# Performance work log

Measured on AMD Instinct MI355X. Metric: run time of the kernel, lower is better.

The kernel has to match this reference:

```python
import jax, jax.numpy as jnp
import numpy as np
from jax import lax

K_NEIGHBORS = 15
LAM = 1.0
EPS = 1e-8


def _cdist(a):
    # Euclidean pairwise distance, safe sqrt (zero diag has zero grad path handled in bwd module too)
    sq = jnp.sum(a * a, axis=1)
    d2 = sq[:, None] + sq[None, :] - 2.0 * (a @ a.T)
    d2 = jnp.maximum(d2, 0.0)
    safe = jnp.where(d2 > 0.0, d2, 1.0)
    return jnp.where(d2 > 0.0, jnp.sqrt(safe), 0.0)


def _knn_loss(z, x, k):
    B = x.shape[0]
    x_dist = _cdist(x)
    z_dist = _cdist(z)
    eye = jnp.eye(B, dtype=bool)
    x_ns = jnp.where(eye, jnp.inf, x_dist)  # fill_diagonal_(inf)
    _, knn_idx = lax.top_k(-x_ns, k)        # k smallest per row
    mask = jnp.zeros((B, B), dtype=bool).at[jnp.arange(B)[:, None], knn_idx].set(True)
    mask = mask | mask.T
    x_max = jnp.max(jnp.where(mask, x_dist, -jnp.inf))
    z_max = jnp.max(jnp.where(mask, z_dist, -jnp.inf))
    x_norm = x_dist / (x_max + EPS)
    z_norm = z_dist / (z_max + EPS)
    diff2 = (z_norm - x_norm) ** 2
    # mean over masked entries == masked_select(...).mean()
    return jnp.sum(jnp.where(mask, diff2, 0.0)) / jnp.sum(mask).astype(diff2.dtype)


def setup_inputs() -> dict:
    key = jax.random.key(0)
    ks = jax.random.split(key, 13)
    D, H1, H2, L = 1024, 2048, 512, 64

    def lin(k, fan_in, fan_out):
        bound = 1.0 / np.sqrt(fan_in)
        kw, kb = jax.random.split(k)
        w = jax.random.uniform(kw, (fan_in, fan_out), jnp.float32, -bound, bound)
        b = jax.random.uniform(kb, (fan_out,), jnp.float32, -bound, bound)
        return w, b

    x = jax.random.normal(ks[0], (8192, D), jnp.float32)
    w_e0, b_e0 = lin(ks[1], D, H1)
    w_e1, b_e1 = lin(ks[2], H1, H2)
    w_e2, b_e2 = lin(ks[3], H2, L)
    w_d0, b_d0 = lin(ks[4], L, H2)
    w_d1, b_d1 = lin(ks[5], H2, H1)
    w_d2, b_d2 = lin(ks[6], H1, D)
    return {"x": x,
            "w_e0": w_e0, "b_e0": b_e0, "w_e1": w_e1, "b_e1": b_e1, "w_e2": w_e2, "b_e2": b_e2,
            "w_d0": w_d0, "b_d0": b_d0, "w_d1": w_d1, "b_d1": b_d1, "w_d2": w_d2, "b_d2": b_d2}


def reference(x, w_e0, b_e0, w_e1, b_e1, w_e2, b_e2, w_d0, b_d0, w_d1, b_d1, w_d2, b_d2):
    h = jax.nn.relu(x @ w_e0 + b_e0)
    h = jax.nn.relu(h @ w_e1 + b_e1)
    z = h @ w_e2 + b_e2
    h = jax.nn.relu(z @ w_d0 + b_d0)
    h = jax.nn.relu(h @ w_d1 + b_d1)
    x_rec = h @ w_d2 + b_d2
    rec_loss = jnp.mean((x_rec - x) ** 2)
    knn_loss = _knn_loss(z, x, K_NEIGHBORS)
    total = rec_loss + LAM * knn_loss
    return (total, z, rec_loss, knn_loss)
```

## Files before the change

kernel.cpp:

```cpp
#include <hip/hip_runtime.h>


typedef __attribute__((ext_vector_type(8))) short bf16x8;
typedef __attribute__((ext_vector_type(4))) float f32x4;

#define DEVINL static __device__ __forceinline__

DEVINL unsigned short f2bf(float f){
  unsigned u = __float_as_uint(f);
  u += 0x7FFFu + ((u >> 16) & 1u);
  return (unsigned short)(u >> 16);
}

DEVINL int med3i(int a, int b, int c){
  int d;
  asm("v_med3_i32 %0, %1, %2, %3" : "=v"(d) : "v"(a), "v"(b), "v"(c));
  return d;
}

DEVINL void gload16(const unsigned short* g, void* lds){
  __builtin_amdgcn_global_load_lds(
      (const __attribute__((address_space(1))) unsigned int*)g,
      (__attribute__((address_space(3))) unsigned int*)lds, 16, 0, 0);
}

DEVINL void lds_barrier(){
  asm volatile("s_waitcnt lgkmcnt(0)" ::: "memory");
  __builtin_amdgcn_s_barrier();
  asm volatile("" ::: "memory");
}

#define NLISTS 39

#define INS15(NAME, R0,R1,R2,R3,R4,R5,R6,R7,R8,R9,R10,R11,R12,R13,R14)  \
  auto NAME = [&](int v){                                               \
    if (v < R14){                                                       \
      R14 = med3i(v, R13, R14); R13 = med3i(v, R12, R13);               \
      R12 = med3i(v, R11, R12); R11 = med3i(v, R10, R11);               \
      R10 = med3i(v, R9 , R10); R9  = med3i(v, R8 , R9 );               \
      R8  = med3i(v, R7 , R8 ); R7  = med3i(v, R6 , R7 );               \
      R6  = med3i(v, R5 , R6 ); R5  = med3i(v, R4 , R5 );               \
      R4  = med3i(v, R3 , R4 ); R3  = med3i(v, R2 , R3 );               \
      R2  = med3i(v, R1 , R2 ); R1  = med3i(v, R0 , R1 );               \
      R0  = min(R0, v);                                                 \
    }                                                                   \
  }

__global__ __launch_bounds__(256) void cvtT_k(const float* __restrict__ x,
    unsigned short* __restrict__ xb, float* __restrict__ xsq,
    const float* __restrict__ w0, const float* __restrict__ w1,
    const float* __restrict__ w2, const float* __restrict__ w3,
    const float* __restrict__ w4, const float* __restrict__ w5,
    unsigned short* __restrict__ t0, unsigned short* __restrict__ t1,
    unsigned short* __restrict__ t2, unsigned short* __restrict__ t3,
    unsigned short* __restrict__ t4, unsigned short* __restrict__ t5)
{
  __shared__ float t[32][33];
  const int tid = threadIdx.x;
  if (blockIdx.x >= 2048){
    int id = blockIdx.x - 2048;
    const float* w; unsigned short* wt; int K, N, loc;
    if      (id < 2048){ w = w0; wt = t0; K = 1024; N = 2048; loc = id; }
    else if (id < 3072){ w = w1; wt = t1; K = 2048; N = 512;  loc = id - 2048; }
    else if (id < 3104){ w = w2; wt = t2; K = 512;  N = 64;   loc = id - 3072; }
    else if (id < 3136){ w = w3; wt = t3; K = 64;   N = 512;  loc = id - 3104; }
    else if (id < 4160){ w = w4; wt = t4; K = 512;  N = 2048; loc = id - 3136; }
    else               { w = w5; wt = t5; K = 2048; N = 1024; loc = id - 4160; }
    const int ntn = N >> 5;
    const int n0 = (loc % ntn) << 5, k0 = (loc / ntn) << 5;
    const int tx = tid & 31, ty = tid >> 5;
    #pragma unroll
    for (int q = 0; q < 4; q++)
      t[ty + 8*q][tx] = w[(size_t)(k0 + ty + 8*q) * N + n0 + tx];
    __syncthreads();
    #pragma unroll
    for (int q = 0; q < 4; q++)
      wt[(size_t)(n0 + ty + 8*q) * K + k0 + tx] = f2bf(t[tx][ty + 8*q]);
    return;
  }
  const int lane = tid & 63, wv = tid >> 6;
  const int row = blockIdx.x * 4 + wv;
  const float4* px = (const float4*)(x + (size_t)row * 1024);
  ushort4* pb = (ushort4*)(xb + (size_t)row * 1024);
  float ss = 0.f;
  #pragma unroll
  for (int q = 0; q < 4; q++){
    float4 v = px[q * 64 + lane];
    ss += v.x*v.x + v.y*v.y + v.z*v.z + v.w*v.w;
    ushort4 o; o.x = f2bf(v.x); o.y = f2bf(v.y); o.z = f2bf(v.z); o.w = f2bf(v.w);
    pb[q * 64 + lane] = o;
  }
  #pragma unroll
  for (int o = 32; o; o >>= 1) ss += __shfl_xor(ss, o);
  if (!lane) xsq[row] = ss;
}

__global__ __launch_bounds__(256, 2) void thr_k(
    const unsigned short* __restrict__ Xb, const float* __restrict__ xsq,
    int* __restrict__ thrI)
{
  __shared__ short As[128][32];
  __shared__ unsigned short d2s[128][130];
  const int tid = threadIdx.x, lane = tid & 63, wid = tid >> 6;
  const int wr = wid >> 1, wc = wid & 1;
  const int r16 = lane & 15, kg = lane >> 4;
  const int srow = lane >> 2, scol = (lane & 3) * 8;
  const float INF = __builtin_inff();
  const int b0 = blockIdx.x * 128;

  float xr[4][4];
  #pragma unroll
  for (int m = 0; m < 4; m++)
    #pragma unroll
    for (int r = 0; r < 4; r++)
      xr[m][r] = xsq[b0 + wr*64 + m*16 + kg*4 + r];

  f32x4 acc[4][4] = {};
  for (int k0 = 0; k0 < 1024; k0 += 32){
    __syncthreads();
    for (int ch = wid; ch < 8; ch += 4)
      gload16(Xb + (size_t)(b0 + ch*16 + srow) * 1024 + k0 + scol, &As[ch*16][0]);
    __syncthreads();
    bf16x8 af[4], bfr[4];
    #pragma unroll
    for (int m = 0; m < 4; m++) af[m]  = *(const bf16x8*)&As[wr*64 + m*16 + r16][kg*8];
    #pragma unroll
    for (int n = 0; n < 4; n++) bfr[n] = *(const bf16x8*)&As[wc*64 + n*16 + r16][kg*8];
    #pragma unroll
    for (int m = 0; m < 4; m++)
      #pragma unroll
      for (int n = 0; n < 4; n++)
        acc[m][n] = __builtin_amdgcn_mfma_f32_16x16x32_bf16(af[m], bfr[n], acc[m][n], 0, 0, 0);
  }
  float xc[4];
  #pragma unroll
  for (int n = 0; n < 4; n++) xc[n] = xsq[b0 + wc*64 + n*16 + r16];
  #pragma unroll
  for (int m = 0; m < 4; m++){
    #pragma unroll
    for (int n = 0; n < 4; n++){
      const int lc = wc*64 + n*16 + r16;
      #pragma unroll
      for (int r = 0; r < 4; r++){
        const int lr = wr*64 + m*16 + kg*4 + r;
        float v = xr[m][r] + xc[n] - 2.f * acc[m][n][r];
        if (lr == lc) v = INF;
        d2s[lr][lc] = f2bf(v);
      }
    }
  }
  __syncthreads();
  if (tid < 128){
    int r0,r1,r2,r3,r4,r5,r6,r7,r8,r9,r10,r11,r12,r13,r14;
    r0=r1=r2=r3=r4=r5=r6=r7=r8=r9=r10=r11=r12=r13=r14=0x7FFFFFFF;
    INS15(ins, r0,r1,r2,r3,r4,r5,r6,r7,r8,r9,r10,r11,r12,r13,r14);
    #pragma unroll 4
    for (int cc = 0; cc < 128; cc += 2){
      unsigned pv = *(const unsigned*)&d2s[tid][cc];
      ins((int)((pv << 16) | (unsigned)cc));
      ins((int)((pv & 0xFFFF0000u) | (unsigned)(cc + 1)));
    }
    thrI[b0 + tid] = (int)(((unsigned)r14 & 0xFFFF0000u) | 0xFFFFu);
  }
}

template<int BM, int BN, int WM, int WN, bool RELU, int OMODE>
__global__ __launch_bounds__(256, 2) void gemm_bt(
    const unsigned short* __restrict__ A, const unsigned short* __restrict__ Bt,
    const float* __restrict__ bias, int M, int N, int K,
    unsigned short* __restrict__ Cb, float* __restrict__ Cf,
    const float* __restrict__ Xref, float* __restrict__ recPart)
{
  constexpr int FM = BM / (WM * 16), FN = BN / (WN * 16);
  __shared__ short As[BM][32];
  __shared__ short Bs[BN][32];
  __shared__ float wsum[4];
  const int tid = threadIdx.x, lane = tid & 63, wid = tid >> 6;
  const int wr = wid / WN, wc = wid % WN;
  const int r16 = lane & 15, kg = lane >> 4;
  const int row0 = blockIdx.x * BM, col0 = blockIdx.y * BN;
  const int srow = lane >> 2, scol = (lane & 3) * 8;
  (void)M;
  f32x4 acc[FM][FN] = {};
  for (int k0 = 0; k0 < K; k0 += 32){
    __syncthreads();
    for (int ch = wid; ch < BM/16; ch += 4)
      gload16(A + (size_t)(row0 + ch*16 + srow) * K + k0 + scol, &As[ch*16][0]);
    for (int ch = wid; ch < BN/16; ch += 4)
      gload16(Bt + (size_t)(col0 + ch*16 + srow) * K + k0 + scol, &Bs[ch*16][0]);
    __syncthreads();
    bf16x8 af[FM], bfr[FN];
    #pragma unroll
    for (int m = 0; m < FM; m++) af[m]  = *(const bf16x8*)&As[wr*FM*16 + m*16 + r16][kg*8];
    #pragma unroll
    for (int n = 0; n < FN; n++) bfr[n] = *(const bf16x8*)&Bs[wc*FN*16 + n*16 + r16][kg*8];
    #pragma unroll
    for (int m = 0; m < FM; m++)
      #pragma unroll
      for (int n = 0; n < FN; n++)
        acc[m][n] = __builtin_amdgcn_mfma_f32_16x16x32_bf16(af[m], bfr[n], acc[m][n], 0, 0, 0);
  }
  float lsum = 0.f;
  #pragma unroll
  for (int m = 0; m < FM; m++){
    #pragma unroll
    for (int n = 0; n < FN; n++){
      const int gc = col0 + wc*FN*16 + n*16 + r16;
      const float bv = bias[gc];
      #pragma unroll
      for (int r = 0; r < 4; r++){
        const int gr = row0 + wr*FM*16 + m*16 + kg*4 + r;
        float v = acc[m][n][r] + bv;
        if (RELU) v = fmaxf(v, 0.f);
        if (OMODE == 2){
          float d = v - Xref[(size_t)gr * N + gc];
          lsum += d * d;
        } else {
          Cb[(size_t)gr * N + gc] = f2bf(v);
          if (OMODE == 1) Cf[(size_t)gr * N + gc] = v;
        }
      }
    }
  }
  if (OMODE == 2){
    #pragma unroll
    for (int o = 32; o; o >>= 1) lsum += __shfl_xor(lsum, o);
    if (!lane) wsum[wid] = lsum;
    __syncthreads();
    if (!tid) recPart[blockIdx.y * gridDim.x + blockIdx.x] =
        wsum[0] + wsum[1] + wsum[2] + wsum[3];
  }
}

__global__ __launch_bounds__(256, 2) void gram_topk_k(
    const unsigned short* __restrict__ Xb, const float* __restrict__ xsq,
    const int* __restrict__ thrI, int* __restrict__ topP,
    const unsigned short* __restrict__ gBt, const float* __restrict__ gBias,
    unsigned short* __restrict__ gC)
{
  __shared__ short As[128][32];
  __shared__ short Bs[128][32];
  __shared__ unsigned short d2s[128][130];
  __shared__ int colL[128][15];
  __shared__ unsigned bkt[16][256];
  const int tid = threadIdx.x, lane = tid & 63, wid = tid >> 6;
  const int wr = wid >> 1, wc = wid & 1;
  const int r16 = lane & 15, kg = lane >> 4;
  const int srow = lane >> 2, scol = (lane & 3) * 8;

  if (blockIdx.x >= 512){
    const int gb = blockIdx.x - 512;
    const int row0 = (gb & 63) * 128, col0 = (gb >> 6) * 128;
    f32x4 acc[4][4] = {};
    for (int k0 = 0; k0 < 1024; k0 += 32){
      __syncthreads();
      for (int ch = wid; ch < 8; ch += 4){
        gload16(Xb  + (size_t)(row0 + ch*16 + srow) * 1024 + k0 + scol, &As[ch*16][0]);
        gload16(gBt + (size_t)(col0 + ch*16 + srow) * 1024 + k0 + scol, &Bs[ch*16][0]);
      }
      __syncthreads();
      bf16x8 af[4], bfr[4];
      #pragma unroll
      for (int m = 0; m < 4; m++) af[m]  = *(const bf16x8*)&As[wr*64 + m*16 + r16][kg*8];
      #pragma unroll
      for (int n = 0; n < 4; n++) bfr[n] = *(const bf16x8*)&Bs[wc*64 + n*16 + r16][kg*8];
      #pragma unroll
      for (int m = 0; m < 4; m++)
        #pragma unroll
        for (int n = 0; n < 4; n++)
          acc[m][n] = __builtin_amdgcn_mfma_f32_16x16x32_bf16(af[m], bfr[n], acc[m][n], 0, 0, 0);
    }
    #pragma unroll
    for (int m = 0; m < 4; m++){
      #pragma unroll
      for (int n = 0; n < 4; n++){
        const int gc = col0 + wc*64 + n*16 + r16;
        const float bv = gBias[gc];
        #pragma unroll
        for (int r = 0; r < 4; r++){
          const int gr = row0 + wr*64 + m*16 + kg*4 + r;
          gC[(size_t)gr * 2048 + gc] = f2bf(fmaxf(acc[m][n][r] + bv, 0.f));
        }
      }
    }
    return;
  }

  const float INF = __builtin_inff();
  const int INFI = 0x7FFFFFFF;
  const int bi = blockIdx.x & 63;
  const int cl = blockIdx.x >> 6;
  const int row0 = bi * 128;
  const int ntt = (cl == 7) ? 5 : 4;
  const int selrow = tid & 127, half = tid >> 7, selc0 = half * 64;
  const int thrRI = thrI[row0 + selrow];

  auto stage = [&](int j0s, int k0s){
    for (int ch = wid; ch < 8; ch += 4){
      gload16(Xb + (size_t)(row0 + ch*16 + srow) * 1024 + k0s + scol, &As[ch*16][0]);
      gload16(Xb + (size_t)(j0s  + ch*16 + srow) * 1024 + k0s + scol, &Bs[ch*16][0]);
    }
  };

  int r0,r1,r2,r3,r4,r5,r6,r7,r8,r9,r10,r11,r12,r13,r14;
  r0=r1=r2=r3=r4=r5=r6=r7=r8=r9=r10=r11=r12=r13=r14=INFI;
  INS15(insR, r0,r1,r2,r3,r4,r5,r6,r7,r8,r9,r10,r11,r12,r13,r14);
  int c0,c1,c2,c3,c4,c5,c6,c7,c8,c9,c10,c11,c12,c13,c14;
  INS15(insC, c0,c1,c2,c3,c4,c5,c6,c7,c8,c9,c10,c11,c12,c13,c14);

  float xr[4][4];
  #pragma unroll
  for (int m = 0; m < 4; m++)
    #pragma unroll
    for (int r = 0; r < 4; r++)
      xr[m][r] = xsq[row0 + wr*64 + m*16 + kg*4 + r];

  stage(((bi + cl * 4) & 63) * 128, 0);

  for (int tt = 0; tt < ntt; ++tt){
    const int d = cl * 4 + tt;
    const int bj = (bi + d) & 63;
    const int j0 = bj * 128;
    f32x4 acc[4][4] = {};
    for (int k0 = 0; k0 < 1024; k0 += 32){
      __syncthreads();
      bf16x8 af[4], bfr[4];
      #pragma unroll
      for (int m = 0; m < 4; m++) af[m]  = *(const bf16x8*)&As[wr*64 + m*16 + r16][kg*8];
      #pragma unroll
      for (int n = 0; n < 4; n++) bfr[n] = *(const bf16x8*)&Bs[wc*64 + n*16 + r16][kg*8];
      __syncthreads();
      if (k0 + 32 < 1024)      stage(j0, k0 + 32);
      else if (tt + 1 < ntt)   stage(((bi + d + 1) & 63) * 128, 0);
      #pragma unroll
      for (int m = 0; m < 4; m++)
        #pragma unroll
        for (int n = 0; n < 4; n++)
          acc[m][n] = __builtin_amdgcn_mfma_f32_16x16x32_bf16(af[m], bfr[n], acc[m][n], 0, 0, 0);
    }
    float xc[4];
    #pragma unroll
    for (int n = 0; n < 4; n++) xc[n] = xsq[j0 + wc*64 + n*16 + r16];
    #pragma unroll
    for (int m = 0; m < 4; m++){
      #pragma unroll
      for (int n = 0; n < 4; n++){
        const int lc = wc*64 + n*16 + r16;
        #pragma unroll
        for (int r = 0; r < 4; r++){
          const int lr = wr*64 + m*16 + kg*4 + r;
          float v = xr[m][r] + xc[n] - 2.f * acc[m][n][r];
          if (row0 + lr == j0 + lc) v = INF;
          d2s[lr][lc] = f2bf(v);
        }
      }
    }
    lds_barrier();

    {
      int cnt = 0;
      const int jg0 = j0 + selc0;
      #pragma unroll 4
      for (int cc = 0; cc < 64; cc += 2){
        unsigned pv = *(const unsigned*)&d2s[selrow][selc0 + cc];
        int p0 = (int)((pv << 16) | (unsigned)(jg0 + cc));
        int p1 = (int)((pv & 0xFFFF0000u) | (unsigned)(jg0 + cc + 1));
        if (p0 <= thrRI){
          if (cnt < 16){ bkt[cnt][tid] = (unsigned)p0; ++cnt; } else insR(p0);
        }
        if (p1 <= thrRI){
          if (cnt < 16){ bkt[cnt][tid] = (unsigned)p1; ++cnt; } else insR(p1);
        }
      }
      for (int q = 0; q < cnt; ++q) insR((int)bkt[q][tid]);
    }

    const bool doCol = (d >= 1) && (d <= 31);
    if (doCol){
      c0=c1=c2=c3=c4=c5=c6=c7=c8=c9=c10=c11=c12=c13=c14=INFI;
      const int thrCI = thrI[j0 + selrow];
      const int rbase = row0 + selc0;
      int cnt = 0;
      #pragma unroll 4
      for (int rr = 0; rr < 64; ++rr){
        unsigned v = d2s[selc0 + rr][selrow];
        int pk = (int)((v << 16) | (unsigned)(rbase + rr));
        if (pk <= thrCI){
          if (cnt < 16){ bkt[cnt][tid] = (unsigned)pk; ++cnt; } else insC(pk);
        }
      }
      for (int q = 0; q < cnt; ++q) insC((int)bkt[q][tid]);
      if (half){
        colL[selrow][0]=c0;  colL[selrow][1]=c1;  colL[selrow][2]=c2;
        colL[selrow][3]=c3;  colL[selrow][4]=c4;  colL[selrow][5]=c5;
        colL[selrow][6]=c6;  colL[selrow][7]=c7;  colL[selrow][8]=c8;
        colL[selrow][9]=c9;  colL[selrow][10]=c10; colL[selrow][11]=c11;
        colL[selrow][12]=c12; colL[selrow][13]=c13; colL[selrow][14]=c14;
      }
    }
    lds_barrier();
    if (doCol && !half){
      #pragma unroll 1
      for (int q = 0; q < 15; ++q){
        int v = colL[selrow][q];
        if (v >= c14) break;
        insC(v);
      }
      int* dst = topP + ((size_t)(j0 + selrow) * NLISTS + (8 + d - 1)) * 15;
      dst[0]=c0;  dst[1]=c1;  dst[2]=c2;  dst[3]=c3;  dst[4]=c4;
      dst[5]=c5;  dst[6]=c6;  dst[7]=c7;  dst[8]=c8;  dst[9]=c9;
      dst[10]=c10; dst[11]=c11; dst[12]=c12; dst[13]=c13; dst[14]=c14;
    }
  }
  lds_barrier();
  if (half){
    colL[selrow][0]=r0;  colL[selrow][1]=r1;  colL[selrow][2]=r2;
    colL[selrow][3]=r3;  colL[selrow][4]=r4;  colL[selrow][5]=r5;
    colL[selrow][6]=r6;  colL[selrow][7]=r7;  colL[selrow][8]=r8;
    colL[selrow][9]=r9;  colL[selrow][10]=r10; colL[selrow][11]=r11;
    colL[selrow][12]=r12; colL[selrow][13]=r13; colL[selrow][14]=r14;
  }
  lds_barrier();
  if (!half){
    #pragma unroll 1
    for (int q = 0; q < 15; ++q){
      int v = colL[selrow][q];
      if (v >= r14) break;
      insR(v);
    }
    int* dst = topP + ((size_t)(row0 + selrow) * NLISTS + cl) * 15;
    dst[0]=r0;  dst[1]=r1;  dst[2]=r2;  dst[3]=r3;  dst[4]=r4;
    dst[5]=r5;  dst[6]=r6;  dst[7]=r7;  dst[8]=r8;  dst[9]=r9;
    dst[10]=r10; dst[11]=r11; dst[12]=r12; dst[13]=r13; dst[14]=r14;
  }
}

__global__ __launch_bounds__(256) void merge_topk_k(const int* __restrict__ topP,
    int* __restrict__ knn, float* __restrict__ d2k, float* __restrict__ xpart)
{
  __shared__ float wmax[4];
  const int lane = threadIdx.x & 63, wid = threadIdx.x >> 6;
  const int row = blockIdx.x * 4 + wid;
  const int* tp = topP + (size_t)row * (NLISTS * 15);
  const int INFI = 0x7FFFFFFF;
  int c0 = tp[lane];
  int c1 = tp[lane + 64];
  int c2 = tp[lane + 128];
  int c3 = tp[lane + 192];
  int c4 = tp[lane + 256];
  int c5 = tp[lane + 320];
  int c6 = tp[lane + 384];
  int c7 = tp[lane + 448];
  int c8 = tp[lane + 512];
  int c9 = (lane < 9) ? tp[lane + 576] : INFI;
  float last = 0.f;
  for (int it = 0; it < 15; ++it){
    int m = min(min(min(c0, c1), min(c2, c3)), min(min(c4, c5), min(c6, c7)));
    m = min(m, min(c8, c9));
    #pragma unroll
    for (int o = 32; o; o >>= 1) m = min(m, __shfl_xor(m, o));
    if (!lane){
      knn[row * 15 + it] = m & 0xFFFF;
      float f = __uint_as_float((unsigned)m & 0xFFFF0000u);
      d2k[row * 15 + it] = f;
      last = f;
    }
    c0 = (c0 == m) ? INFI : c0;   c1 = (c1 == m) ? INFI : c1;
    c2 = (c2 == m) ? INFI : c2;   c3 = (c3 == m) ? INFI : c3;
    c4 = (c4 == m) ? INFI : c4;   c5 = (c5 == m) ? INFI : c5;
    c6 = (c6 == m) ? INFI : c6;   c7 = (c7 == m) ? INFI : c7;
    c8 = (c8 == m) ? INFI : c8;   c9 = (c9 == m) ? INFI : c9;
  }
  if (!lane) wmax[wid] = last;
  __syncthreads();
  if (!threadIdx.x)
    xpart[blockIdx.x] = fmaxf(fmaxf(wmax[0], wmax[1]), fmaxf(wmax[2], wmax[3]));
}

__global__ __launch_bounds__(256) void pair_sums_k(
    const float* __restrict__ z, const int* __restrict__ knn,
    const float* __restrict__ d2k,
    float* __restrict__ zzP, float* __restrict__ zxP, float* __restrict__ xxP,
    float* __restrict__ zmP, float* __restrict__ cntP)
{
  __shared__ float red[4][5];
  const int lane = threadIdx.x & 63, wid = threadIdx.x >> 6;
  float szz = 0.f, szx = 0.f, sxx = 0.f, mz = 0.f, scnt = 0.f;
  for (int p = blockIdx.x * 4 + wid; p < 122880; p += gridDim.x * 4){
    const int i = p / 15;
    const int j = knn[p];
    const float dx2 = d2k[p];
    float dd = z[(size_t)i * 64 + lane] - z[(size_t)j * 64 + lane];
    float s = dd * dd;
    #pragma unroll
    for (int o = 32; o; o >>= 1) s += __shfl_xor(s, o);
    int kj = knn[j * 15 + min(lane, 14)];
    unsigned long long m2 = __ballot(lane < 15 && kj == i);
    const float w = m2 ? 1.f : 2.f;
    float dz = sqrtf(s), dx = sqrtf(dx2);
    szz += w * s;
    szx += w * dz * dx;
    sxx += w * dx2;
    scnt += w;
    mz = fmaxf(mz, dz);
  }
  if (!lane){
    red[wid][0] = szz; red[wid][1] = szx; red[wid][2] = sxx;
    red[wid][3] = mz;  red[wid][4] = scnt;
  }
  __syncthreads();
  if (!threadIdx.x){
    float a = 0.f, b = 0.f, c = 0.f, m = 0.f, n = 0.f;
    #pragma unroll
    for (int w = 0; w < 4; w++){
      a += red[w][0]; b += red[w][1]; c += red[w][2];
      m = fmaxf(m, red[w][3]); n += red[w][4];
    }
    zzP[blockIdx.x] = a; zxP[blockIdx.x] = b; xxP[blockIdx.x] = c;
    zmP[blockIdx.x] = m; cntP[blockIdx.x] = n;
  }
}

__global__ __launch_bounds__(256) void final_reduce_k(
    const float* __restrict__ recPart, const float* __restrict__ xpart,
    const float* __restrict__ zzP, const float* __restrict__ zxP,
    const float* __restrict__ xxP, const float* __restrict__ zmP,
    const float* __restrict__ cntP, float* __restrict__ out)
{
  __shared__ float rd[4][7];
  const int t = threadIdx.x, lane = t & 63, wid = t >> 6;
  float rec = 0.f, xm = 0.f, zz = 0.f, zx = 0.f, xx = 0.f, zm = 0.f, cnt = 0.f;
  for (int i = t; i < 1024; i += 256) rec += recPart[i];
  for (int i = t; i < 2048; i += 256) xm = fmaxf(xm, xpart[i]);
  for (int i = t; i < 1920; i += 256){
    zz += zzP[i]; zx += zxP[i]; xx += xxP[i]; cnt += cntP[i];
    zm = fmaxf(zm, zmP[i]);
  }
  #pragma unroll
  for (int o = 32; o; o >>= 1){
    rec += __shfl_xor(rec, o); zz += __shfl_xor(zz, o);
    zx  += __shfl_xor(zx, o);  xx += __shfl_xor(xx, o);
    cnt += __shfl_xor(cnt, o);
    xm = fmaxf(xm, __shfl_xor(xm, o));
    zm = fmaxf(zm, __shfl_xor(zm, o));
  }
  if (!lane){
    rd[wid][0]=rec; rd[wid][1]=zz; rd[wid][2]=zx; rd[wid][3]=xx;
    rd[wid][4]=xm;  rd[wid][5]=zm; rd[wid][6]=cnt;
  }
  __syncthreads();
  if (!t){
    rec = rd[0][0]+rd[1][0]+rd[2][0]+rd[3][0];
    zz  = rd[0][1]+rd[1][1]+rd[2][1]+rd[3][1];
    zx  = rd[0][2]+rd[1][2]+rd[2][2]+rd[3][2];
    xx  = rd[0][3]+rd[1][3]+rd[2][3]+rd[3][3];
    xm  = fmaxf(fmaxf(rd[0][4],rd[1][4]), fmaxf(rd[2][4],rd[3][4]));
    zm  = fmaxf(fmaxf(rd[0][5],rd[1][5]), fmaxf(rd[2][5],rd[3][5]));
    cnt = rd[0][6]+rd[1][6]+rd[2][6]+rd[3][6];
    rec *= 1.0f / (8192.0f * 1024.0f);
    float xmax = sqrtf(xm);
    float rx = 1.0f / (xmax + 1e-8f), rz = 1.0f / (zm + 1e-8f);
    float knn = (zz * rz * rz - 2.0f * zx * rz * rx + xx * rx * rx) / cnt;
    out[0] = rec + knn;
    out[1 + 8192 * 64]     = rec;
    out[1 + 8192 * 64 + 1] = knn;
  }
}

extern "C" void kernel_launch(void* const* d_in, const int* in_sizes, int n_in,
                              void* d_out, int out_size, void* d_ws, size_t ws_size,
                              hipStream_t stream)
{
  (void)in_sizes; (void)n_in; (void)out_size;
  const float* x    = (const float*)d_in[0];
  const float* w_e0 = (const float*)d_in[1];  const float* b_e0 = (const float*)d_in[2];
  const float* w_e1 = (const float*)d_in[3];  const float* b_e1 = (const float*)d_in[4];
  const float* w_e2 = (const float*)d_in[5];  const float* b_e2 = (const float*)d_in[6];
  const float* w_d0 = (const float*)d_in[7];  const float* b_d0 = (const float*)d_in[8];
  const float* w_d1 = (const float*)d_in[9];  const float* b_d1 = (const float*)d_in[10];
  const float* w_d2 = (const float*)d_in[11]; const float* b_d2 = (const float*)d_in[12];
  float* out = (float*)d_out;

  char* ws = (char*)d_ws;
  size_t off = 0;
  auto alloc = [&](size_t bytes) -> void* {
    void* p = ws + off;
    off += (bytes + 255) & ~(size_t)255;
    return p;
  };
  unsigned short* xb   = (unsigned short*)alloc(8192ull * 1024 * 2);
  unsigned short* wte0 = (unsigned short*)alloc(2048ull * 1024 * 2);
  unsigned short* wte1 = (unsigned short*)alloc(512ull  * 2048 * 2);
  unsigned short* wte2 = (unsigned short*)alloc(64ull   * 512  * 2);
  unsigned short* wtd0 = (unsigned short*)alloc(512ull  * 64   * 2);
  unsigned short* wtd1 = (unsigned short*)alloc(2048ull * 512  * 2);
  unsigned short* wtd2 = (unsigned short*)alloc(1024ull * 2048 * 2);
  unsigned short* bufA = (unsigned short*)alloc(8192ull * 2048 * 2);
  unsigned short* bufB = (unsigned short*)alloc(8192ull * 512  * 2);
  unsigned short* zb   = (unsigned short*)alloc(8192ull * 64   * 2);
  int*   topP   = (int*)  alloc(8192ull * NLISTS * 15 * 4);
  float* xsq    = (float*)alloc(8192 * 4);
  int*   thrI   = (int*)  alloc(8192 * 4);
  int*   knn    = (int*)  alloc(8192ull * 15 * 4);
  float* d2k    = (float*)alloc(8192ull * 15 * 4);
  float* xpart  = (float*)alloc(2048 * 4);
  float* zzP    = (float*)alloc(1920 * 4);
  float* zxP    = (float*)alloc(1920 * 4);
  float* xxP    = (float*)alloc(1920 * 4);
  float* zmP    = (float*)alloc(1920 * 4);
  float* cntP   = (float*)alloc(1920 * 4);
  float* recPart= (float*)alloc(1024 * 4);
  if (off > ws_size) return;

  cvtT_k<<<8256, 256, 0, stream>>>(x, xb, xsq,
      w_e0, w_e1, w_e2, w_d0, w_d1, w_d2, wte0, wte1, wte2, wtd0, wtd1, wtd2);

  thr_k<<<64, 256, 0, stream>>>(xb, xsq, thrI);

  gram_topk_k<<<1536, 256, 0, stream>>>(xb, xsq, thrI, topP, wte0, b_e0, bufA);
  merge_topk_k<<<2048, 256, 0, stream>>>(topP, knn, d2k, xpart);

  gemm_bt<128, 64,2,2,true ,0><<<dim3(64, 8), 256, 0, stream>>>(bufA, wte1, b_e1, 8192,  512, 2048, bufB, nullptr, nullptr, nullptr);
  gemm_bt< 32, 64,2,2,false,1><<<dim3(256,1), 256, 0, stream>>>(bufB, wte2, b_e2, 8192,   64,  512, zb,   out + 1, nullptr, nullptr);
  gemm_bt<128, 64,2,2,true ,0><<<dim3(64, 8), 256, 0, stream>>>(zb,   wtd0, b_d0, 8192,  512,   64, bufB, nullptr, nullptr, nullptr);
  gemm_bt<128,128,2,2,true ,0><<<dim3(64,16), 256, 0, stream>>>(bufB, wtd1, b_d1, 8192, 2048,  512, bufA, nullptr, nullptr, nullptr);
  gemm_bt< 64,128,2,2,false,2><<<dim3(128,8), 256, 0, stream>>>(bufA, wtd2, b_d2, 8192, 1024, 2048, nullptr, nullptr, x, recPart);

  pair_sums_k<<<1920, 256, 0, stream>>>(out + 1, knn, d2k, zzP, zxP, xxP, zmP, cntP);
  final_reduce_k<<<1, 256, 0, stream>>>(recPart, xpart, zzP, zxP, xxP, zmP, cntP, out);
}
```

Measured before the change: 418.7 us.

## Filter kNN candidates in GEMM epilogue via LDS atomic queues

Moves threshold filtering of row and column kNN candidates into the Gram-tile epilogue, where each accumulator element is tested and pushed into per-row and per-column LDS queues with atomic counters. Row and column selection are then split across the two thread halves, dropping the two-half partial lists and their merge barriers. If a queue overflows, that row or column falls back to a full rescan of the tile. This removes the strided rescans of the d2s tile but adds LDS atomics in the epilogue and makes per-thread work uneven.

Result: slower. 448.0 us (+7.0%).

```diff
diff --git a/kernel.cpp b/kernel.cpp
--- a/kernel.cpp
+++ b/kernel.cpp
@@ -31,6 +31,7 @@
 }
 
 #define NLISTS 39
+#define QCAP   24
 
 #define INS15(NAME, R0,R1,R2,R3,R4,R5,R6,R7,R8,R9,R10,R11,R12,R13,R14)  \
   auto NAME = [&](int v){                                               \
@@ -241,8 +242,10 @@
   __shared__ short As[128][32];
   __shared__ short Bs[128][32];
   __shared__ unsigned short d2s[128][130];
-  __shared__ int colL[128][15];
-  __shared__ unsigned bkt[16][256];
+  __shared__ unsigned rowQ[128][QCAP];
+  __shared__ unsigned colQ[128][QCAP];
+  __shared__ int qcR[128];
+  __shared__ int qcC[128];
   const int tid = threadIdx.x, lane = tid & 63, wid = tid >> 6;
   const int wr = wid >> 1, wc = wid & 1;
   const int r16 = lane & 15, kg = lane >> 4;
@@ -292,8 +295,6 @@
   const int cl = blockIdx.x >> 6;
   const int row0 = bi * 128;
   const int ntt = (cl == 7) ? 5 : 4;
-  const int selrow = tid & 127, half = tid >> 7, selc0 = half * 64;
-  const int thrRI = thrI[row0 + selrow];
 
   auto stage = [&](int j0s, int k0s){
     for (int ch = wid; ch < 8; ch += 4){
@@ -304,16 +305,19 @@
 
   int r0,r1,r2,r3,r4,r5,r6,r7,r8,r9,r10,r11,r12,r13,r14;
   r0=r1=r2=r3=r4=r5=r6=r7=r8=r9=r10=r11=r12=r13=r14=INFI;
-  INS15(insR, r0,r1,r2,r3,r4,r5,r6,r7,r8,r9,r10,r11,r12,r13,r14);
-  int c0,c1,c2,c3,c4,c5,c6,c7,c8,c9,c10,c11,c12,c13,c14;
-  INS15(insC, c0,c1,c2,c3,c4,c5,c6,c7,c8,c9,c10,c11,c12,c13,c14);
-
-  float xr[4][4];
+  INS15(ins, r0,r1,r2,r3,r4,r5,r6,r7,r8,r9,r10,r11,r12,r13,r14);
+
+  float xr[4][4]; int thrR[4][4];
   #pragma unroll
   for (int m = 0; m < 4; m++)
     #pragma unroll
-    for (int r = 0; r < 4; r++)
-      xr[m][r] = xsq[row0 + wr*64 + m*16 + kg*4 + r];
+    for (int r = 0; r < 4; r++){
+      const int gr = row0 + wr*64 + m*16 + kg*4 + r;
+      xr[m][r] = xsq[gr];
+      thrR[m][r] = thrI[gr];
+    }
+
+  if (tid < 128) qcR[tid] = 0; else qcC[tid - 128] = 0;
 
   stage(((bi + cl * 4) & 63) * 128, 0);
 
@@ -321,6 +325,7 @@
     const int d = cl * 4 + tt;
     const int bj = (bi + d) & 63;
     const int j0 = bj * 128;
+    const bool doCol = (d >= 1) && (d <= 31);
     f32x4 acc[4][4] = {};
     for (int k0 = 0; k0 < 1024; k0 += 32){
       __syncthreads();
@@ -338,9 +343,13 @@
         for (int n = 0; n < 4; n++)
           acc[m][n] = __builtin_amdgcn_mfma_f32_16x16x32_bf16(af[m], bfr[n], acc[m][n], 0, 0, 0);
     }
-    float xc[4];
-    #pragma unroll
-    for (int n = 0; n < 4; n++) xc[n] = xsq[j0 + wc*64 + n*16 + r16];
+    float xc[4]; int thrCl[4];
+    #pragma unroll
+    for (int n = 0; n < 4; n++){
+      const int lc = wc*64 + n*16 + r16;
+      xc[n] = xsq[j0 + lc];
+      thrCl[n] = doCol ? thrI[j0 + lc] : (int)0x80000000;
+    }
     #pragma unroll
     for (int m = 0; m < 4; m++){
       #pragma unroll
@@ -351,84 +360,57 @@
           const int lr = wr*64 + m*16 + kg*4 + r;
           float v = xr[m][r] + xc[n] - 2.f * acc[m][n][r];
           if (row0 + lr == j0 + lc) v = INF;
-          d2s[lr][lc] = f2bf(v);
+          const unsigned short bf = f2bf(v);
+          d2s[lr][lc] = bf;
+          const int pk = (int)(((unsigned)bf << 16) | (unsigned)(j0 + lc));
+          if (pk <= thrR[m][r]){
+            int s = atomicAdd(&qcR[lr], 1);
+            if (s < QCAP) rowQ[lr][s] = (unsigned)pk;
+          }
+          const int pc = (int)(((unsigned)bf << 16) | (unsigned)(row0 + lr));
+          if (pc <= thrCl[n]){
+            int s = atomicAdd(&qcC[lc], 1);
+            if (s < QCAP) colQ[lc][s] = (unsigned)pc;
+          }
         }
       }
     }
     lds_barrier();
 
-    {
-      int cnt = 0;
-      const int jg0 = j0 + selc0;
-      #pragma unroll 4
-      for (int cc = 0; cc < 64; cc += 2){
-        unsigned pv = *(const unsigned*)&d2s[selrow][selc0 + cc];
-        int p0 = (int)((pv << 16) | (unsigned)(jg0 + cc));
-        int p1 = (int)((pv & 0xFFFF0000u) | (unsigned)(jg0 + cc + 1));
-        if (p0 <= thrRI){
-          if (cnt < 16){ bkt[cnt][tid] = (unsigned)p0; ++cnt; } else insR(p0);
-        }
-        if (p1 <= thrRI){
-          if (cnt < 16){ bkt[cnt][tid] = (unsigned)p1; ++cnt; } else insR(p1);
+    if (tid < 128){
+      const int cnt = qcR[tid];
+      if (cnt <= QCAP){
+        for (int q = 0; q < cnt; ++q) ins((int)rowQ[tid][q]);
+      } else {
+        #pragma unroll 4
+        for (int cc = 0; cc < 128; cc += 2){
+          unsigned pv = *(const unsigned*)&d2s[tid][cc];
+          ins((int)((pv << 16) | (unsigned)(j0 + cc)));
+          ins((int)((pv & 0xFFFF0000u) | (unsigned)(j0 + cc + 1)));
         }
       }
-      for (int q = 0; q < cnt; ++q) insR((int)bkt[q][tid]);
-    }
-
-    const bool doCol = (d >= 1) && (d <= 31);
-    if (doCol){
-      c0=c1=c2=c3=c4=c5=c6=c7=c8=c9=c10=c11=c12=c13=c14=INFI;
-      const int thrCI = thrI[j0 + selrow];
-      const int rbase = row0 + selc0;
-      int cnt = 0;
-      #pragma unroll 4
-      for (int rr = 0; rr < 64; ++rr){
-        unsigned v = d2s[selc0 + rr][selrow];
-        int pk = (int)((v << 16) | (unsigned)(rbase + rr));
-        if (pk <= thrCI){
-          if (cnt < 16){ bkt[cnt][tid] = (unsigned)pk; ++cnt; } else insC(pk);
+    } else if (doCol){
+      const int c = tid - 128;
+      r0=r1=r2=r3=r4=r5=r6=r7=r8=r9=r10=r11=r12=r13=r14=INFI;
+      const int cnt = qcC[c];
+      if (cnt <= QCAP){
+        for (int q = 0; q < cnt; ++q) ins((int)colQ[c][q]);
+      } else {
+        for (int rr = 0; rr < 128; ++rr){
+          unsigned v = d2s[rr][c];
+          ins((int)((v << 16) | (unsigned)(row0 + rr)));
         }
       }
-      for (int q = 0; q < cnt; ++q) insC((int)bkt[q][tid]);
-      if (half){
-        colL[selrow][0]=c0;  colL[selrow][1]=c1;  colL[selrow][2]=c2;
-        colL[selrow][3]=c3;  colL[selrow][4]=c4;  colL[selrow][5]=c5;
-        colL[selrow][6]=c6;  colL[selrow][7]=c7;  colL[selrow][8]=c8;
-        colL[selrow][9]=c9;  colL[selrow][10]=c10; colL[selrow][11]=c11;
-        colL[selrow][12]=c12; colL[selrow][13]=c13; colL[selrow][14]=c14;
-      }
+      int* dst = topP + ((size_t)(j0 + c) * NLISTS + (8 + d - 1)) * 15;
+      dst[0]=r0;  dst[1]=r1;  dst[2]=r2;  dst[3]=r3;  dst[4]=r4;
+      dst[5]=r5;  dst[6]=r6;  dst[7]=r7;  dst[8]=r8;  dst[9]=r9;
+      dst[10]=r10; dst[11]=r11; dst[12]=r12; dst[13]=r13; dst[14]=r14;
     }
     lds_barrier();
-    if (doCol && !half){
-      #pragma unroll 1
-      for (int q = 0; q < 15; ++q){
-        int v = colL[selrow][q];
-        if (v >= c14) break;
-        insC(v);
-      }
-      int* dst = topP + ((size_t)(j0 + selrow) * NLISTS + (8 + d - 1)) * 15;
-      dst[0]=c0;  dst[1]=c1;  dst[2]=c2;  dst[3]=c3;  dst[4]=c4;
-      dst[5]=c5;  dst[6]=c6;  dst[7]=c7;  dst[8]=c8;  dst[9]=c9;
-      dst[10]=c10; dst[11]=c11; dst[12]=c12; dst[13]=c13; dst[14]=c14;
-    }
-  }
-  lds_barrier();
-  if (half){
-    colL[selrow][0]=r0;  colL[selrow][1]=r1;  colL[selrow][2]=r2;
-    colL[selrow][3]=r3;  colL[selrow][4]=r4;  colL[selrow][5]=r5;
-    colL[selrow][6]=r6;  colL[selrow][7]=r7;  colL[selrow][8]=r8;
-    colL[selrow][9]=r9;  colL[selrow][10]=r10; colL[selrow][11]=r11;
-    colL[selrow][12]=r12; colL[selrow][13]=r13; colL[selrow][14]=r14;
-  }
-  lds_barrier();
-  if (!half){
-    #pragma unroll 1
-    for (int q = 0; q < 15; ++q){
-      int v = colL[selrow][q];
-      if (v >= r14) break;
-      insR(v);
-    }
-    int* dst = topP + ((size_t)(row0 + selrow) * NLISTS + cl) * 15;
+    if (tid < 128) qcR[tid] = 0; else qcC[tid - 128] = 0;
+  }
+  if (tid < 128){
+    int* dst = topP + ((size_t)(row0 + tid) * NLISTS + cl) * 15;
     dst[0]=r0;  dst[1]=r1;  dst[2]=r2;  dst[3]=r3;  dst[4]=r4;
     dst[5]=r5;  dst[6]=r6;  dst[7]=r7;  dst[8]=r8;  dst[9]=r9;
     dst[10]=r10; dst[11]=r11; dst[12]=r12; dst[13]=r13; dst[14]=r14;
```
